# Optimization experiments

Measured on AMD Instinct MI355X. Metric: run time of the kernel, lower is better.

The kernel has to match this reference:

```python
import jax, jax.numpy as jnp
import numpy as np

B, N, C, H = 8, 1024, 768, 12
D = C // H
SCALE = D ** -0.5


def setup_inputs() -> dict:
    key = jax.random.key(0)
    ks = jax.random.split(key, 6)
    std = 0.02
    return {
        "x": jax.random.normal(ks[0], (B, N, C), dtype=jnp.float32),
        "w_qkv": jax.random.normal(ks[1], (3 * C, C), dtype=jnp.float32) * std,
        "w_proj": jax.random.normal(ks[2], (C, C), dtype=jnp.float32) * std,
        "b_proj": jnp.zeros((C,), dtype=jnp.float32),
        "conv_l_w": jax.random.normal(ks[3], (H, H), dtype=jnp.float32) * std,
        "conv_w_w": jax.random.normal(ks[4], (H, H), dtype=jnp.float32) * std,
    }


def reference(x, w_qkv, w_proj, b_proj, conv_l_w, conv_w_w):
    Bx, Nx, Cx = x.shape
    # qkv projection: torch Linear uses x @ W^T
    qkv = (x @ w_qkv.T).reshape(Bx, Nx, 3, H, D)
    qkv = jnp.transpose(qkv, (2, 0, 3, 1, 4))  # [3, B, H, N, D]
    q, k, v = qkv[0], qkv[1], qkv[2]
    q = q * SCALE
    attn = jnp.einsum("bhnd,bhmd->bhnm", q, k)  # [B,H,N,N]
    # 1x1 conv across heads (conv_l)
    attn = jnp.einsum("oh,bhnm->bonm", conv_l_w, attn)
    attn = jax.nn.softmax(attn, axis=-1)
    # 1x1 conv across heads (conv_w)
    attn = jnp.einsum("oh,bhnm->bonm", conv_w_w, attn)
    out = jnp.einsum("bhnm,bhmd->bhnd", attn, v)
    out = jnp.transpose(out, (0, 2, 1, 3)).reshape(Bx, Nx, Cx)
    return out @ w_proj.T + b_proj
```

## Files before the change

### kernel.cpp

```cpp
#include <hip/hip_runtime.h>
#include <hip/hip_bf16.h>

typedef __attribute__((ext_vector_type(8))) short short8;
typedef __attribute__((ext_vector_type(4))) short short4v;
typedef __attribute__((ext_vector_type(4))) float float4v;

#define NB 8
#define NH 12
#define NN 1024
#define ND 64
#define NC 768

#define RAWBAR() do { \
  asm volatile("s_waitcnt lgkmcnt(0)" ::: "memory"); \
  __builtin_amdgcn_s_barrier(); \
} while (0)

__device__ __forceinline__ short f2bf(float f) {
  __hip_bfloat16 h = __float2bfloat16(f);
  union { __hip_bfloat16 h; short s; } u; u.h = h; return u.s;
}
__device__ __forceinline__ unsigned pk2(float a, float b) {
  unsigned ua = (unsigned short)f2bf(a);
  unsigned ub = (unsigned short)f2bf(b);
  return ua | (ub << 16);
}

template<int MODE>
__global__ __launch_bounds__(256, 2)
void gemm_kernel(const void* __restrict__ Ap, const float* __restrict__ Bw,
                 const float* __restrict__ bias,
                 __hip_bfloat16* __restrict__ Qo, __hip_bfloat16* __restrict__ Ko,
                 __hip_bfloat16* __restrict__ VTo, float* __restrict__ Out)
{
  __shared__ short As[128 * 40];
  __shared__ short Bs[128 * 40];
  const int tid = threadIdx.x;
  const int w = tid >> 6, lane = tid & 63, lr = lane & 15, lg = lane >> 4;
  const int wr = w >> 1, wc = w & 1;
  const int n0 = blockIdx.x * 128, m0 = blockIdx.y * 128;

  float4v acc[4][4];
  #pragma unroll
  for (int i = 0; i < 4; i++)
    #pragma unroll
    for (int j = 0; j < 4; j++)
      acc[i][j] = (float4v){0.f, 0.f, 0.f, 0.f};

  for (int kt = 0; kt < 768; kt += 32) {
    if (MODE == 0) {
      const float* A = (const float*)Ap;
      #pragma unroll
      for (int i2 = 0; i2 < 4; i2++) {
        int c = tid + 256 * i2;
        int row = c >> 3, c4 = c & 7;
        float4v v = *(const float4v*)(A + (size_t)(m0 + row) * 768 + kt + c4 * 4);
        short4v s = { f2bf(v[0]), f2bf(v[1]), f2bf(v[2]), f2bf(v[3]) };
        *(short4v*)(&As[row * 40 + c4 * 4]) = s;
      }
    } else {
      const __hip_bfloat16* A = (const __hip_bfloat16*)Ap;
      #pragma unroll
      for (int i2 = 0; i2 < 2; i2++) {
        int c = tid + 256 * i2;
        int row = c >> 2, c8 = c & 3;
        *(short8*)(&As[row * 40 + c8 * 8]) =
            *(const short8*)(A + (size_t)(m0 + row) * 768 + kt + c8 * 8);
      }
    }
    #pragma unroll
    for (int i2 = 0; i2 < 4; i2++) {
      int c = tid + 256 * i2;
      int row = c >> 3, c4 = c & 7;
      float4v v = *(const float4v*)(Bw + (size_t)(n0 + row) * 768 + kt + c4 * 4);
      short4v s = { f2bf(v[0]), f2bf(v[1]), f2bf(v[2]), f2bf(v[3]) };
      *(short4v*)(&Bs[row * 40 + c4 * 4]) = s;
    }
    __syncthreads();

    short8 af[4], bfr[4];
    #pragma unroll
    for (int i = 0; i < 4; i++)
      af[i] = *(const short8*)(&As[(wr * 64 + i * 16 + lr) * 40 + lg * 8]);
    #pragma unroll
    for (int j = 0; j < 4; j++)
      bfr[j] = *(const short8*)(&Bs[(wc * 64 + j * 16 + lr) * 40 + lg * 8]);
    #pragma unroll
    for (int i = 0; i < 4; i++)
      #pragma unroll
      for (int j = 0; j < 4; j++)
        acc[i][j] = __builtin_amdgcn_mfma_f32_16x16x32_bf16(af[i], bfr[j], acc[i][j], 0, 0, 0);
    __syncthreads();
  }

  #pragma unroll
  for (int i = 0; i < 4; i++) {
    #pragma unroll
    for (int j = 0; j < 4; j++) {
      #pragma unroll
      for (int r = 0; r < 4; r++) {
        float val = acc[i][j][r];
        int mg_ = m0 + wr * 64 + i * 16 + lg * 4 + r;
        int ng_ = n0 + wc * 64 + j * 16 + lr;
        if (MODE == 0) {
          int s = ng_ / 768;
          int rem = ng_ - s * 768;
          int h = rem >> 6, d = rem & 63;
          int b = mg_ >> 10, n = mg_ & 1023;
          if (s == 0)
            Qo[(((size_t)b * NH + h) * NN + n) * ND + d] = __float2bfloat16(val * 0.125f);
          else if (s == 1)
            Ko[(((size_t)b * NH + h) * NN + n) * ND + d] = __float2bfloat16(val);
          else
            VTo[(((size_t)b * NH + h) * ND + d) * NN + n] = __float2bfloat16(val);
        } else {
          Out[(size_t)mg_ * NC + ng_] = val + bias[ng_];
        }
      }
    }
  }
}

__global__ __launch_bounds__(256, 2)
void attn_kernel(const __hip_bfloat16* __restrict__ Qg, const __hip_bfloat16* __restrict__ Kg,
                 const __hip_bfloat16* __restrict__ VTg,
                 const float* __restrict__ convl, const float* __restrict__ convw,
                 __hip_bfloat16* __restrict__ AOut)
{
  __shared__ short Sb[18432];
  __shared__ short pm[18688];
  __shared__ short lwA[512];
  __shared__ short wwT[512];

  const int tid = threadIdx.x;
  const int w = tid >> 6, lane = tid & 63, lr = lane & 15, lg = lane >> 4;
  const int b = blockIdx.x & 7;
  const int n0 = (blockIdx.x >> 3) * 16;
  const float4v zf = (float4v){0.f, 0.f, 0.f, 0.f};

  for (int i = tid; i < 512; i += 256) {
    int r = i >> 5, k = i & 31;
    bool v = (r < 12) && (k < 12);
    lwA[i] = v ? f2bf(convl[r * 12 + k]) : (short)0;
    wwT[i] = v ? f2bf(convw[r * 12 + k]) : (short)0;
  }
  for (int i = tid; i < 1024; i += 256) {
    unsigned* p = (unsigned*)(&Sb[i * 18 + 12]);
    p[0] = 0; p[1] = 0; p[2] = 0;
  }

  short8 qf[3][2];
  #pragma unroll
  for (int hh = 0; hh < 3; hh++)
    #pragma unroll
    for (int ks = 0; ks < 2; ks++)
      qf[hh][ks] = *(const short8*)(Qg +
          (((size_t)b * NH + w * 3 + hh) * NN + n0 + lr) * ND + ks * 32 + lg * 8);

  short8 kreg[3][2][2];
  auto loadK = [&](int t) {
    #pragma unroll
    for (int hh = 0; hh < 3; hh++) {
      const size_t kbase = (((size_t)b * NH + w * 3 + hh) * NN + t * 32) * ND;
      #pragma unroll
      for (int j = 0; j < 2; j++)
        #pragma unroll
        for (int ks = 0; ks < 2; ks++)
          kreg[hh][j][ks] = *(const short8*)(Kg + kbase +
              (size_t)(j * 16 + lr) * ND + ks * 32 + lg * 8);
    }
  };

  auto qkStep = [&](int buf) {
    #pragma unroll
    for (int hh = 0; hh < 3; hh++) {
      const int h = w * 3 + hh;
      #pragma unroll
      for (int j = 0; j < 2; j++) {
        float4v a = __builtin_amdgcn_mfma_f32_16x16x32_bf16(qf[hh][0], kreg[hh][j][0], zf, 0, 0, 0);
        a = __builtin_amdgcn_mfma_f32_16x16x32_bf16(qf[hh][1], kreg[hh][j][1], a, 0, 0, 0);
        #pragma unroll
        for (int r = 0; r < 4; r++)
          Sb[(buf * 32 + (lg * 4 + r) * 2 + j) * 288 + lr * 18 + h] = f2bf(a[r]);
      }
    }
  };

  loadK(0);
  RAWBAR();
  const short8 lwf = *(const short8*)(&lwA[lr * 32 + lg * 8]);
  const short8 wwf = *(const short8*)(&wwT[lr * 32 + lg * 8]);

  float Lacc[4][4];
  #pragma unroll
  for (int r = 0; r < 4; r++)
    #pragma unroll
    for (int nn = 0; nn < 4; nn++) Lacc[r][nn] = 0.f;

  for (int t = 0; t <= 32; t++) {
    __builtin_amdgcn_s_setprio(1);
    if (t < 32) qkStep(t & 1);
    __builtin_amdgcn_s_setprio(0);
    if (t < 32) loadK(t < 31 ? t + 1 : 0);
    if (t >= 1) {
      const int buf = (t - 1) & 1;
      #pragma unroll
      for (int cc = 0; cc < 8; cc++) {
        const int c = w * 8 + cc;
        short8 sb = *(const short8*)(&Sb[(buf * 32 + c) * 288 + lr * 18 + lg * 8]);
        float4v d = __builtin_amdgcn_mfma_f32_16x16x32_bf16(lwf, sb, zf, 0, 0, 0);
        #pragma unroll
        for (int r = 0; r < 4; r++)
          Lacc[r][cc >> 1] += __expf(d[r]);
      }
    }
    RAWBAR();
  }
  float logLreg[4][4];
  #pragma unroll
  for (int r = 0; r < 4; r++)
    #pragma unroll
    for (int nn = 0; nn < 4; nn++) {
      float v = Lacc[r][nn];
      v += __shfl_xor(v, 1);
      v += __shfl_xor(v, 2);
      v += __shfl_xor(v, 4);
      v += __shfl_xor(v, 8);
      logLreg[r][nn] = __logf(v);
    }

  float4v oacc[3][4];
  #pragma unroll
  for (int hh = 0; hh < 3; hh++)
    #pragma unroll
    for (int jd = 0; jd < 4; jd++) oacc[hh][jd] = zf;

  for (int t = 0; t <= 33; t++) {
    short8 pf[3];
    short8 vt[3][4];
    if (t >= 2) {
      const int pb = t & 1;
      const int m0v = (t - 2) * 32;
      #pragma unroll
      for (int hh = 0; hh < 3; hh++) {
        const int o2 = w * 3 + hh;
        pf[hh] = *(const short8*)(&pm[pb * 9344 + o2 * 584 + lr * 36 + lg * 8]);
        const size_t vbase = ((size_t)b * NH + o2) * ND * NN;
        #pragma unroll
        for (int jd = 0; jd < 4; jd++)
          vt[hh][jd] = *(const short8*)(VTg + vbase +
              (size_t)(jd * 16 + lr) * NN + m0v + lg * 8);
      }
    }
    __builtin_amdgcn_s_setprio(1);
    if (t < 32) {
      qkStep(t & 1);
      if (t < 31) loadK(t + 1);
    }
    __builtin_amdgcn_s_setprio(0);
    if (t >= 1 && t <= 32) {
      const int buf = (t - 1) & 1;
      #pragma unroll
      for (int cc = 0; cc < 8; cc++) {
        const int c = w * 8 + cc;
        short8 sb = *(const short8*)(&Sb[(buf * 32 + c) * 288 + lr * 18 + lg * 8]);
        float4v d = __builtin_amdgcn_mfma_f32_16x16x32_bf16(lwf, sb, zf, 0, 0, 0);
        float p0 = __expf(d[0] - logLreg[0][cc >> 1]);
        float p1 = __expf(d[1] - logLreg[1][cc >> 1]);
        float p2 = __expf(d[2] - logLreg[2][cc >> 1]);
        float p3 = __expf(d[3] - logLreg[3][cc >> 1]);
        unsigned* dst = (unsigned*)(&Sb[(buf * 32 + c) * 288 + lr * 18 + lg * 4]);
        dst[0] = pk2(p0, p1);
        dst[1] = pk2(p2, p3);
      }
      asm volatile("s_waitcnt lgkmcnt(0)" ::: "memory");
      __builtin_amdgcn_sched_barrier(0);
      #pragma unroll
      for (int cc = 0; cc < 8; cc++) {
        const int c = w * 8 + cc;
        short8 pb2 = *(const short8*)(&Sb[(buf * 32 + c) * 288 + lr * 18 + lg * 8]);
        float4v d = __builtin_amdgcn_mfma_f32_16x16x32_bf16(pb2, wwf, zf, 0, 0, 0);
        unsigned* dst = (unsigned*)(&pm[buf * 9344 + lr * 584 + (c >> 1) * 36 + (c & 1) * 16 + lg * 4]);
        dst[0] = pk2(d[0], d[1]);
        dst[1] = pk2(d[2], d[3]);
      }
    }
    if (t >= 2) {
      __builtin_amdgcn_s_setprio(1);
      #pragma unroll
      for (int hh = 0; hh < 3; hh++)
        #pragma unroll
        for (int jd = 0; jd < 4; jd++)
          oacc[hh][jd] = __builtin_amdgcn_mfma_f32_16x16x32_bf16(vt[hh][jd], pf[hh], oacc[hh][jd], 0, 0, 0);
      __builtin_amdgcn_s_setprio(0);
    }
    RAWBAR();
  }

  #pragma unroll
  for (int hh = 0; hh < 3; hh++) {
    const int o2 = w * 3 + hh;
    #pragma unroll
    for (int jd = 0; jd < 4; jd++) {
      size_t base = ((size_t)b * NN + n0 + lr) * NC + o2 * 64 + jd * 16 + lg * 4;
      unsigned* dst = (unsigned*)(&AOut[base]);
      dst[0] = pk2(oacc[hh][jd][0], oacc[hh][jd][1]);
      dst[1] = pk2(oacc[hh][jd][2], oacc[hh][jd][3]);
    }
  }
}

extern "C" void kernel_launch(void* const* d_in, const int* in_sizes, int n_in,
                              void* d_out, int out_size, void* d_ws, size_t ws_size,
                              hipStream_t stream) {
  const float* x      = (const float*)d_in[0];
  const float* w_qkv  = (const float*)d_in[1];
  const float* w_proj = (const float*)d_in[2];
  const float* b_proj = (const float*)d_in[3];
  const float* conv_l = (const float*)d_in[4];
  const float* conv_w = (const float*)d_in[5];
  float* out = (float*)d_out;

  const size_t NE = (size_t)NB * NH * NN * ND;
  __hip_bfloat16* Qb = (__hip_bfloat16*)d_ws;
  __hip_bfloat16* Kb = Qb + NE;
  __hip_bfloat16* VT = Kb + NE;
  __hip_bfloat16* AO = VT + NE;

  gemm_kernel<0><<<dim3(18, 64), 256, 0, stream>>>(x, w_qkv, nullptr, Qb, Kb, VT, nullptr);
  attn_kernel<<<dim3(512), 256, 0, stream>>>(Qb, Kb, VT, conv_l, conv_w, AO);
  gemm_kernel<1><<<dim3(6, 64), 256, 0, stream>>>(AO, w_proj, b_proj, nullptr, nullptr, nullptr, out);
}
```

Baseline: 377.0 us.

## Process 64-key tiles in first attention pass using a unified shared buffer

```diff
diff --git a/kernel.cpp b/kernel.cpp
--- a/kernel.cpp
+++ b/kernel.cpp
@@ -127,10 +127,11 @@
                  const float* __restrict__ convl, const float* __restrict__ convw,
                  __hip_bfloat16* __restrict__ AOut)
 {
-  __shared__ short Sb[18432];
-  __shared__ short pm[18688];
+  __shared__ short SMEM[37376];
   __shared__ short lwA[512];
   __shared__ short wwT[512];
+  short* Sb = SMEM;
+  short* pm = SMEM + 18688;
 
   const int tid = threadIdx.x;
   const int w = tid >> 6, lane = tid & 63, lr = lane & 15, lg = lane >> 4;
@@ -144,10 +145,7 @@
     lwA[i] = v ? f2bf(convl[r * 12 + k]) : (short)0;
     wwT[i] = v ? f2bf(convw[r * 12 + k]) : (short)0;
   }
-  for (int i = tid; i < 1024; i += 256) {
-    unsigned* p = (unsigned*)(&Sb[i * 18 + 12]);
-    p[0] = 0; p[1] = 0; p[2] = 0;
-  }
+  for (int i = tid; i < 18688; i += 256) ((unsigned*)SMEM)[i] = 0u;
 
   short8 qf[3][2];
   #pragma unroll
@@ -158,31 +156,16 @@
           (((size_t)b * NH + w * 3 + hh) * NN + n0 + lr) * ND + ks * 32 + lg * 8);
 
   short8 kreg[3][2][2];
-  auto loadK = [&](int t) {
+  auto loadK = [&](int mbase) {
     #pragma unroll
     for (int hh = 0; hh < 3; hh++) {
-      const size_t kbase = (((size_t)b * NH + w * 3 + hh) * NN + t * 32) * ND;
+      const size_t kbase = (((size_t)b * NH + w * 3 + hh) * NN + mbase) * ND;
       #pragma unroll
       for (int j = 0; j < 2; j++)
         #pragma unroll
         for (int ks = 0; ks < 2; ks++)
           kreg[hh][j][ks] = *(const short8*)(Kg + kbase +
               (size_t)(j * 16 + lr) * ND + ks * 32 + lg * 8);
-    }
-  };
-
-  auto qkStep = [&](int buf) {
-    #pragma unroll
-    for (int hh = 0; hh < 3; hh++) {
-      const int h = w * 3 + hh;
-      #pragma unroll
-      for (int j = 0; j < 2; j++) {
-        float4v a = __builtin_amdgcn_mfma_f32_16x16x32_bf16(qf[hh][0], kreg[hh][j][0], zf, 0, 0, 0);
-        a = __builtin_amdgcn_mfma_f32_16x16x32_bf16(qf[hh][1], kreg[hh][j][1], a, 0, 0, 0);
-        #pragma unroll
-        for (int r = 0; r < 4; r++)
-          Sb[(buf * 32 + (lg * 4 + r) * 2 + j) * 288 + lr * 18 + h] = f2bf(a[r]);
-      }
     }
   };
 
@@ -197,21 +180,51 @@
     #pragma unroll
     for (int nn = 0; nn < 4; nn++) Lacc[r][nn] = 0.f;
 
-  for (int t = 0; t <= 32; t++) {
+  for (int t = 0; t <= 16; t++) {
     __builtin_amdgcn_s_setprio(1);
-    if (t < 32) qkStep(t & 1);
+    if (t < 16) {
+      const int buf = (t & 1) * 64;
+      const int mt = t * 64;
+      #pragma unroll
+      for (int hh = 0; hh < 3; hh++) {
+        const int h = w * 3 + hh;
+        #pragma unroll
+        for (int j = 0; j < 2; j++) {
+          float4v a = __builtin_amdgcn_mfma_f32_16x16x32_bf16(qf[hh][0], kreg[hh][j][0], zf, 0, 0, 0);
+          a = __builtin_amdgcn_mfma_f32_16x16x32_bf16(qf[hh][1], kreg[hh][j][1], a, 0, 0, 0);
+          #pragma unroll
+          for (int r = 0; r < 4; r++)
+            Sb[(buf + ((lg * 4 + r) * 4 + j)) * 292 + lr * 18 + h] = f2bf(a[r]);
+        }
+      }
+      #pragma unroll
+      for (int hh = 0; hh < 3; hh++) {
+        const int h = w * 3 + hh;
+        const size_t kbase = (((size_t)b * NH + h) * NN + mt + 32) * ND;
+        #pragma unroll
+        for (int j = 0; j < 2; j++) {
+          short8 kb0 = *(const short8*)(Kg + kbase + (size_t)(j * 16 + lr) * ND + lg * 8);
+          short8 kb1 = *(const short8*)(Kg + kbase + (size_t)(j * 16 + lr) * ND + 32 + lg * 8);
+          float4v a = __builtin_amdgcn_mfma_f32_16x16x32_bf16(qf[hh][0], kb0, zf, 0, 0, 0);
+          a = __builtin_amdgcn_mfma_f32_16x16x32_bf16(qf[hh][1], kb1, a, 0, 0, 0);
+          #pragma unroll
+          for (int r = 0; r < 4; r++)
+            Sb[(buf + ((lg * 4 + r) * 4 + 2 + j)) * 292 + lr * 18 + h] = f2bf(a[r]);
+        }
+      }
+      loadK(t < 15 ? (t + 1) * 64 : 0);
+    }
     __builtin_amdgcn_s_setprio(0);
-    if (t < 32) loadK(t < 31 ? t + 1 : 0);
     if (t >= 1) {
-      const int buf = (t - 1) & 1;
-      #pragma unroll
-      for (int cc = 0; cc < 8; cc++) {
-        const int c = w * 8 + cc;
-        short8 sb = *(const short8*)(&Sb[(buf * 32 + c) * 288 + lr * 18 + lg * 8]);
+      const int buf = ((t - 1) & 1) * 64;
+      #pragma unroll
+      for (int cc = 0; cc < 16; cc++) {
+        const int c = w * 16 + cc;
+        short8 sb = *(const short8*)(&Sb[(buf + c) * 292 + lr * 18 + lg * 8]);
         float4v d = __builtin_amdgcn_mfma_f32_16x16x32_bf16(lwf, sb, zf, 0, 0, 0);
         #pragma unroll
         for (int r = 0; r < 4; r++)
-          Lacc[r][cc >> 1] += __expf(d[r]);
+          Lacc[r][cc >> 2] += __expf(d[r]);
       }
     }
     RAWBAR();
@@ -239,12 +252,12 @@
     short8 pf[3];
     short8 vt[3][4];
     if (t >= 2) {
-      const int pb = t & 1;
+      const int pb = (t & 1) * 9344;
       const int m0v = (t - 2) * 32;
       #pragma unroll
       for (int hh = 0; hh < 3; hh++) {
         const int o2 = w * 3 + hh;
-        pf[hh] = *(const short8*)(&pm[pb * 9344 + o2 * 584 + lr * 36 + lg * 8]);
+        pf[hh] = *(const short8*)(&pm[pb + o2 * 584 + lr * 36 + lg * 8]);
         const size_t vbase = ((size_t)b * NH + o2) * ND * NN;
         #pragma unroll
         for (int jd = 0; jd < 4; jd++)
@@ -254,22 +267,34 @@
     }
     __builtin_amdgcn_s_setprio(1);
     if (t < 32) {
-      qkStep(t & 1);
-      if (t < 31) loadK(t + 1);
+      const int buf = (t & 1) * 32;
+      #pragma unroll
+      for (int hh = 0; hh < 3; hh++) {
+        const int h = w * 3 + hh;
+        #pragma unroll
+        for (int j = 0; j < 2; j++) {
+          float4v a = __builtin_amdgcn_mfma_f32_16x16x32_bf16(qf[hh][0], kreg[hh][j][0], zf, 0, 0, 0);
+          a = __builtin_amdgcn_mfma_f32_16x16x32_bf16(qf[hh][1], kreg[hh][j][1], a, 0, 0, 0);
+          #pragma unroll
+          for (int r = 0; r < 4; r++)
+            Sb[(buf + ((lg * 4 + r) * 2 + j)) * 292 + lr * 18 + h] = f2bf(a[r]);
+        }
+      }
+      if (t < 31) loadK((t + 1) * 32);
     }
     __builtin_amdgcn_s_setprio(0);
     if (t >= 1 && t <= 32) {
-      const int buf = (t - 1) & 1;
+      const int buf = ((t - 1) & 1) * 32;
       #pragma unroll
       for (int cc = 0; cc < 8; cc++) {
         const int c = w * 8 + cc;
-        short8 sb = *(const short8*)(&Sb[(buf * 32 + c) * 288 + lr * 18 + lg * 8]);
+        short8 sb = *(const short8*)(&Sb[(buf + c) * 292 + lr * 18 + lg * 8]);
         float4v d = __builtin_amdgcn_mfma_f32_16x16x32_bf16(lwf, sb, zf, 0, 0, 0);
         float p0 = __expf(d[0] - logLreg[0][cc >> 1]);
         float p1 = __expf(d[1] - logLreg[1][cc >> 1]);
         float p2 = __expf(d[2] - logLreg[2][cc >> 1]);
         float p3 = __expf(d[3] - logLreg[3][cc >> 1]);
-        unsigned* dst = (unsigned*)(&Sb[(buf * 32 + c) * 288 + lr * 18 + lg * 4]);
+        unsigned* dst = (unsigned*)(&Sb[(buf + c) * 292 + lr * 18 + lg * 4]);
         dst[0] = pk2(p0, p1);
         dst[1] = pk2(p2, p3);
       }
@@ -278,9 +303,10 @@
       #pragma unroll
       for (int cc = 0; cc < 8; cc++) {
         const int c = w * 8 + cc;
-        short8 pb2 = *(const short8*)(&Sb[(buf * 32 + c) * 288 + lr * 18 + lg * 8]);
+        short8 pb2 = *(const short8*)(&Sb[(buf + c) * 292 + lr * 18 + lg * 8]);
         float4v d = __builtin_amdgcn_mfma_f32_16x16x32_bf16(pb2, wwf, zf, 0, 0, 0);
-        unsigned* dst = (unsigned*)(&pm[buf * 9344 + lr * 584 + (c >> 1) * 36 + (c & 1) * 16 + lg * 4]);
+        unsigned* dst = (unsigned*)(&pm[((t - 1) & 1) * 9344 + lr * 584 +
+                                        (c >> 1) * 36 + (c & 1) * 16 + lg * 4]);
         dst[0] = pk2(d[0], d[1]);
         dst[1] = pk2(d[2], d[3]);
       }
```

Measured after the change: 409.0 us. 1.08x slower.

## Double-buffer K and V register prefetch and pad score buffer rows

Applied to the files above, without the earlier changes.

```diff
diff --git a/kernel.cpp b/kernel.cpp
--- a/kernel.cpp
+++ b/kernel.cpp
@@ -127,7 +127,7 @@
                  const float* __restrict__ convl, const float* __restrict__ convw,
                  __hip_bfloat16* __restrict__ AOut)
 {
-  __shared__ short Sb[18432];
+  __shared__ short Sb[18688];
   __shared__ short pm[18688];
   __shared__ short lwA[512];
   __shared__ short wwT[512];
@@ -144,10 +144,12 @@
     lwA[i] = v ? f2bf(convl[r * 12 + k]) : (short)0;
     wwT[i] = v ? f2bf(convw[r * 12 + k]) : (short)0;
   }
-  for (int i = tid; i < 1024; i += 256) {
-    unsigned* p = (unsigned*)(&Sb[i * 18 + 12]);
-    p[0] = 0; p[1] = 0; p[2] = 0;
-  }
+  for (int i = tid; i < 9344; i += 256) { ((unsigned*)Sb)[i] = 0u; ((unsigned*)pm)[i] = 0u; }
+
+  const int klane = lr * ND + lg * 8;
+  const int vlane = lr * NN + lg * 8;
+  const __hip_bfloat16* Kw = Kg + (((size_t)b * NH + w * 3) * NN) * ND;
+  const __hip_bfloat16* Vw = VTg + (((size_t)b * NH + w * 3) * ND) * NN;
 
   short8 qf[3][2];
   #pragma unroll
@@ -157,36 +159,42 @@
       qf[hh][ks] = *(const short8*)(Qg +
           (((size_t)b * NH + w * 3 + hh) * NN + n0 + lr) * ND + ks * 32 + lg * 8);
 
-  short8 kreg[3][2][2];
-  auto loadK = [&](int t) {
-    #pragma unroll
-    for (int hh = 0; hh < 3; hh++) {
-      const size_t kbase = (((size_t)b * NH + w * 3 + hh) * NN + t * 32) * ND;
+  short8 KA[3][2][2], KB[3][2][2];
+  short8 VA[3][4], VB[3][4];
+
+  auto loadK = [&](int mbase, short8 (&KD)[3][2][2]) {
+    #pragma unroll
+    for (int hh = 0; hh < 3; hh++)
       #pragma unroll
       for (int j = 0; j < 2; j++)
         #pragma unroll
         for (int ks = 0; ks < 2; ks++)
-          kreg[hh][j][ks] = *(const short8*)(Kg + kbase +
-              (size_t)(j * 16 + lr) * ND + ks * 32 + lg * 8);
-    }
-  };
-
-  auto qkStep = [&](int buf) {
+          KD[hh][j][ks] = *(const short8*)(Kw + hh * (NN * ND) +
+              (mbase + j * 16) * ND + ks * 32 + klane);
+  };
+  auto loadVT = [&](int m0v, short8 (&VD)[3][4]) {
+    #pragma unroll
+    for (int hh = 0; hh < 3; hh++)
+      #pragma unroll
+      for (int jd = 0; jd < 4; jd++)
+        VD[hh][jd] = *(const short8*)(Vw + hh * (ND * NN) + jd * 16 * NN + m0v + vlane);
+  };
+  auto qkStep = [&](int bufc, short8 (&KC)[3][2][2]) {
     #pragma unroll
     for (int hh = 0; hh < 3; hh++) {
       const int h = w * 3 + hh;
       #pragma unroll
       for (int j = 0; j < 2; j++) {
-        float4v a = __builtin_amdgcn_mfma_f32_16x16x32_bf16(qf[hh][0], kreg[hh][j][0], zf, 0, 0, 0);
-        a = __builtin_amdgcn_mfma_f32_16x16x32_bf16(qf[hh][1], kreg[hh][j][1], a, 0, 0, 0);
+        float4v a = __builtin_amdgcn_mfma_f32_16x16x32_bf16(qf[hh][0], KC[hh][j][0], zf, 0, 0, 0);
+        a = __builtin_amdgcn_mfma_f32_16x16x32_bf16(qf[hh][1], KC[hh][j][1], a, 0, 0, 0);
         #pragma unroll
         for (int r = 0; r < 4; r++)
-          Sb[(buf * 32 + (lg * 4 + r) * 2 + j) * 288 + lr * 18 + h] = f2bf(a[r]);
+          Sb[(bufc + (lg * 4 + r) * 2 + j) * 292 + lr * 18 + h] = f2bf(a[r]);
       }
     }
   };
 
-  loadK(0);
+  loadK(0, KA);
   RAWBAR();
   const short8 lwf = *(const short8*)(&lwA[lr * 32 + lg * 8]);
   const short8 wwf = *(const short8*)(&wwT[lr * 32 + lg * 8]);
@@ -197,25 +205,33 @@
     #pragma unroll
     for (int nn = 0; nn < 4; nn++) Lacc[r][nn] = 0.f;
 
-  for (int t = 0; t <= 32; t++) {
+  auto convSum = [&](int parity) {
+    const int bufc = parity * 32;
+    #pragma unroll
+    for (int cc = 0; cc < 8; cc++) {
+      const int c = w * 8 + cc;
+      short8 sb = *(const short8*)(&Sb[(bufc + c) * 292 + lr * 18 + lg * 8]);
+      float4v d = __builtin_amdgcn_mfma_f32_16x16x32_bf16(lwf, sb, zf, 0, 0, 0);
+      #pragma unroll
+      for (int r = 0; r < 4; r++)
+        Lacc[r][cc >> 1] += __expf(d[r]);
+    }
+  };
+  auto p1seg = [&](int T, short8 (&KC)[3][2][2], short8 (&KN)[3][2][2]) {
+    loadK(T < 31 ? (T + 1) * 32 : 0, KN);
     __builtin_amdgcn_s_setprio(1);
-    if (t < 32) qkStep(t & 1);
+    qkStep((T & 1) * 32, KC);
     __builtin_amdgcn_s_setprio(0);
-    if (t < 32) loadK(t < 31 ? t + 1 : 0);
-    if (t >= 1) {
-      const int buf = (t - 1) & 1;
-      #pragma unroll
-      for (int cc = 0; cc < 8; cc++) {
-        const int c = w * 8 + cc;
-        short8 sb = *(const short8*)(&Sb[(buf * 32 + c) * 288 + lr * 18 + lg * 8]);
-        float4v d = __builtin_amdgcn_mfma_f32_16x16x32_bf16(lwf, sb, zf, 0, 0, 0);
-        #pragma unroll
-        for (int r = 0; r < 4; r++)
-          Lacc[r][cc >> 1] += __expf(d[r]);
-      }
-    }
+    if (T >= 1) convSum((T - 1) & 1);
     RAWBAR();
-  }
+  };
+  for (int tp = 0; tp < 32; tp += 2) {
+    p1seg(tp, KA, KB);
+    p1seg(tp + 1, KB, KA);
+  }
+  convSum(1);
+  RAWBAR();
+
   float logLreg[4][4];
   #pragma unroll
   for (int r = 0; r < 4; r++)
@@ -235,66 +251,63 @@
     #pragma unroll
     for (int jd = 0; jd < 4; jd++) oacc[hh][jd] = zf;
 
-  for (int t = 0; t <= 33; t++) {
+  auto stream2 = [&](int tau) {
+    const int bufc = (tau & 1) * 32;
+    const int pmb = (tau & 1) * 9344;
+    #pragma unroll
+    for (int cc = 0; cc < 8; cc++) {
+      const int c = w * 8 + cc;
+      short8 sb = *(const short8*)(&Sb[(bufc + c) * 292 + lr * 18 + lg * 8]);
+      float4v d = __builtin_amdgcn_mfma_f32_16x16x32_bf16(lwf, sb, zf, 0, 0, 0);
+      float p0 = __expf(d[0] - logLreg[0][cc >> 1]);
+      float p1 = __expf(d[1] - logLreg[1][cc >> 1]);
+      float p2 = __expf(d[2] - logLreg[2][cc >> 1]);
+      float p3 = __expf(d[3] - logLreg[3][cc >> 1]);
+      unsigned* dst = (unsigned*)(&Sb[(bufc + c) * 292 + lr * 18 + lg * 4]);
+      dst[0] = pk2(p0, p1);
+      dst[1] = pk2(p2, p3);
+    }
+    asm volatile("s_waitcnt lgkmcnt(0)" ::: "memory");
+    __builtin_amdgcn_sched_barrier(0);
+    #pragma unroll
+    for (int cc = 0; cc < 8; cc++) {
+      const int c = w * 8 + cc;
+      short8 pb2 = *(const short8*)(&Sb[(bufc + c) * 292 + lr * 18 + lg * 8]);
+      float4v d = __builtin_amdgcn_mfma_f32_16x16x32_bf16(pb2, wwf, zf, 0, 0, 0);
+      unsigned* dst = (unsigned*)(&pm[pmb + lr * 584 + (c >> 1) * 36 + (c & 1) * 16 + lg * 4]);
+      dst[0] = pk2(d[0], d[1]);
+      dst[1] = pk2(d[2], d[3]);
+    }
+  };
+
+  auto p2seg = [&](int T, short8 (&VLD)[3][4], short8 (&VUSE)[3][4]) {
     short8 pf[3];
-    short8 vt[3][4];
-    if (t >= 2) {
-      const int pb = t & 1;
-      const int m0v = (t - 2) * 32;
-      #pragma unroll
-      for (int hh = 0; hh < 3; hh++) {
-        const int o2 = w * 3 + hh;
-        pf[hh] = *(const short8*)(&pm[pb * 9344 + o2 * 584 + lr * 36 + lg * 8]);
-        const size_t vbase = ((size_t)b * NH + o2) * ND * NN;
-        #pragma unroll
-        for (int jd = 0; jd < 4; jd++)
-          vt[hh][jd] = *(const short8*)(VTg + vbase +
-              (size_t)(jd * 16 + lr) * NN + m0v + lg * 8);
-      }
-    }
+    if (T >= 2) {
+      const int pmb = (T & 1) * 9344;
+      #pragma unroll
+      for (int hh = 0; hh < 3; hh++)
+        pf[hh] = *(const short8*)(&pm[pmb + (w * 3 + hh) * 584 + lr * 36 + lg * 8]);
+    }
+    if (T >= 1 && T <= 32) loadVT((T - 1) * 32, VLD);
     __builtin_amdgcn_s_setprio(1);
-    if (t < 32) {
-      qkStep(t & 1);
-      if (t < 31) loadK(t + 1);
-    }
+    if (T < 32) qkStep((T & 1) * 32, KA);
     __builtin_amdgcn_s_setprio(0);
-    if (t >= 1 && t <= 32) {
-      const int buf = (t - 1) & 1;
-      #pragma unroll
-      for (int cc = 0; cc < 8; cc++) {
-        const int c = w * 8 + cc;
-        short8 sb = *(const short8*)(&Sb[(buf * 32 + c) * 288 + lr * 18 + lg * 8]);
-        float4v d = __builtin_amdgcn_mfma_f32_16x16x32_bf16(lwf, sb, zf, 0, 0, 0);
-        float p0 = __expf(d[0] - logLreg[0][cc >> 1]);
-        float p1 = __expf(d[1] - logLreg[1][cc >> 1]);
-        float p2 = __expf(d[2] - logLreg[2][cc >> 1]);
-        float p3 = __expf(d[3] - logLreg[3][cc >> 1]);
-        unsigned* dst = (unsigned*)(&Sb[(buf * 32 + c) * 288 + lr * 18 + lg * 4]);
-        dst[0] = pk2(p0, p1);
-        dst[1] = pk2(p2, p3);
-      }
-      asm volatile("s_waitcnt lgkmcnt(0)" ::: "memory");
-      __builtin_amdgcn_sched_barrier(0);
-      #pragma unroll
-      for (int cc = 0; cc < 8; cc++) {
-        const int c = w * 8 + cc;
-        short8 pb2 = *(const short8*)(&Sb[(buf * 32 + c) * 288 + lr * 18 + lg * 8]);
-        float4v d = __builtin_amdgcn_mfma_f32_16x16x32_bf16(pb2, wwf, zf, 0, 0, 0);
-        unsigned* dst = (unsigned*)(&pm[buf * 9344 + lr * 584 + (c >> 1) * 36 + (c & 1) * 16 + lg * 4]);
-        dst[0] = pk2(d[0], d[1]);
-        dst[1] = pk2(d[2], d[3]);
-      }
-    }
-    if (t >= 2) {
+    if (T < 31) loadK((T + 1) * 32, KA);
+    if (T >= 1 && T <= 32) stream2(T - 1);
+    if (T >= 2) {
       __builtin_amdgcn_s_setprio(1);
       #pragma unroll
       for (int hh = 0; hh < 3; hh++)
         #pragma unroll
         for (int jd = 0; jd < 4; jd++)
-          oacc[hh][jd] = __builtin_amdgcn_mfma_f32_16x16x32_bf16(vt[hh][jd], pf[hh], oacc[hh][jd], 0, 0, 0);
+          oacc[hh][jd] = __builtin_amdgcn_mfma_f32_16x16x32_bf16(VUSE[hh][jd], pf[hh], oacc[hh][jd], 0, 0, 0);
       __builtin_amdgcn_s_setprio(0);
     }
     RAWBAR();
+  };
+  for (int tp = 0; tp < 34; tp += 2) {
+    p2seg(tp, VB, VA);
+    p2seg(tp + 1, VA, VB);
   }
 
   #pragma unroll
```

Result: slower. 438.8 us (+16.4%).

## Split attention into L-pass and PV-pass kernels, storing exp scores in workspace

Applied to the files above, without the earlier changes.

```diff
diff --git a/kernel.cpp b/kernel.cpp
--- a/kernel.cpp
+++ b/kernel.cpp
@@ -4,6 +4,7 @@
 typedef __attribute__((ext_vector_type(8))) short short8;
 typedef __attribute__((ext_vector_type(4))) short short4v;
 typedef __attribute__((ext_vector_type(4))) float float4v;
+typedef __attribute__((ext_vector_type(2))) unsigned uint2v;
 
 #define NB 8
 #define NH 12
@@ -122,15 +123,12 @@
 }
 
 __global__ __launch_bounds__(256, 2)
-void attn_kernel(const __hip_bfloat16* __restrict__ Qg, const __hip_bfloat16* __restrict__ Kg,
-                 const __hip_bfloat16* __restrict__ VTg,
-                 const float* __restrict__ convl, const float* __restrict__ convw,
-                 __hip_bfloat16* __restrict__ AOut)
+void attn_l_kernel(const __hip_bfloat16* __restrict__ Qg, const __hip_bfloat16* __restrict__ Kg,
+                   const float* __restrict__ convl,
+                   short* __restrict__ Pg, float* __restrict__ Lg)
 {
-  __shared__ short Sb[18432];
-  __shared__ short pm[18688];
+  __shared__ short Sb[18688];
   __shared__ short lwA[512];
-  __shared__ short wwT[512];
 
   const int tid = threadIdx.x;
   const int w = tid >> 6, lane = tid & 63, lr = lane & 15, lg = lane >> 4;
@@ -140,14 +138,9 @@
 
   for (int i = tid; i < 512; i += 256) {
     int r = i >> 5, k = i & 31;
-    bool v = (r < 12) && (k < 12);
-    lwA[i] = v ? f2bf(convl[r * 12 + k]) : (short)0;
-    wwT[i] = v ? f2bf(convw[r * 12 + k]) : (short)0;
-  }
-  for (int i = tid; i < 1024; i += 256) {
-    unsigned* p = (unsigned*)(&Sb[i * 18 + 12]);
-    p[0] = 0; p[1] = 0; p[2] = 0;
-  }
+    lwA[i] = (r < 12 && k < 12) ? f2bf(convl[r * 12 + k]) : (short)0;
+  }
+  for (int i = tid; i < 9344; i += 256) ((unsigned*)Sb)[i] = 0u;
 
   short8 qf[3][2];
   #pragma unroll
@@ -171,25 +164,11 @@
     }
   };
 
-  auto qkStep = [&](int buf) {
-    #pragma unroll
-    for (int hh = 0; hh < 3; hh++) {
-      const int h = w * 3 + hh;
-      #pragma unroll
-      for (int j = 0; j < 2; j++) {
-        float4v a = __builtin_amdgcn_mfma_f32_16x16x32_bf16(qf[hh][0], kreg[hh][j][0], zf, 0, 0, 0);
-        a = __builtin_amdgcn_mfma_f32_16x16x32_bf16(qf[hh][1], kreg[hh][j][1], a, 0, 0, 0);
-        #pragma unroll
-        for (int r = 0; r < 4; r++)
-          Sb[(buf * 32 + (lg * 4 + r) * 2 + j) * 288 + lr * 18 + h] = f2bf(a[r]);
-      }
-    }
-  };
+  short* Pblk = Pg + (size_t)blockIdx.x * 32 * 6144;
 
   loadK(0);
   RAWBAR();
   const short8 lwf = *(const short8*)(&lwA[lr * 32 + lg * 8]);
-  const short8 wwf = *(const short8*)(&wwT[lr * 32 + lg * 8]);
 
   float Lacc[4][4];
   #pragma unroll
@@ -199,24 +178,45 @@
 
   for (int t = 0; t <= 32; t++) {
     __builtin_amdgcn_s_setprio(1);
-    if (t < 32) qkStep(t & 1);
+    if (t < 32) {
+      const int bufc = (t & 1) * 32;
+      #pragma unroll
+      for (int hh = 0; hh < 3; hh++) {
+        const int h = w * 3 + hh;
+        #pragma unroll
+        for (int j = 0; j < 2; j++) {
+          float4v a = __builtin_amdgcn_mfma_f32_16x16x32_bf16(qf[hh][0], kreg[hh][j][0], zf, 0, 0, 0);
+          a = __builtin_amdgcn_mfma_f32_16x16x32_bf16(qf[hh][1], kreg[hh][j][1], a, 0, 0, 0);
+          #pragma unroll
+          for (int r = 0; r < 4; r++)
+            Sb[(bufc + (lg * 4 + r) * 2 + j) * 292 + lr * 18 + h] = f2bf(a[r]);
+        }
+      }
+      if (t < 31) loadK(t + 1);
+    }
     __builtin_amdgcn_s_setprio(0);
-    if (t < 32) loadK(t < 31 ? t + 1 : 0);
     if (t >= 1) {
-      const int buf = (t - 1) & 1;
+      const int bufc = ((t - 1) & 1) * 32;
+      short* Pt = Pblk + (size_t)(t - 1) * 6144;
       #pragma unroll
       for (int cc = 0; cc < 8; cc++) {
         const int c = w * 8 + cc;
-        short8 sb = *(const short8*)(&Sb[(buf * 32 + c) * 288 + lr * 18 + lg * 8]);
+        short8 sb = *(const short8*)(&Sb[(bufc + c) * 292 + lr * 18 + lg * 8]);
         float4v d = __builtin_amdgcn_mfma_f32_16x16x32_bf16(lwf, sb, zf, 0, 0, 0);
-        #pragma unroll
-        for (int r = 0; r < 4; r++)
-          Lacc[r][cc >> 1] += __expf(d[r]);
+        float e0 = __expf(d[0]), e1 = __expf(d[1]);
+        float e2 = __expf(d[2]), e3 = __expf(d[3]);
+        Lacc[0][cc >> 1] += e0; Lacc[1][cc >> 1] += e1;
+        Lacc[2][cc >> 1] += e2; Lacc[3][cc >> 1] += e3;
+        if (lg < 3) {
+          uint2v st = { pk2(e0, e1), pk2(e2, e3) };
+          int soff = (lg < 2) ? (lr * 8 + lg * 4) : (128 + lr * 4);
+          *(uint2v*)(Pt + (size_t)c * 192 + soff) = st;
+        }
       }
     }
     RAWBAR();
   }
-  float logLreg[4][4];
+
   #pragma unroll
   for (int r = 0; r < 4; r++)
     #pragma unroll
@@ -226,8 +226,58 @@
       v += __shfl_xor(v, 2);
       v += __shfl_xor(v, 4);
       v += __shfl_xor(v, 8);
-      logLreg[r][nn] = __logf(v);
-    }
+      int o = lg * 4 + r;
+      if (lr == 0 && o < 12)
+        Lg[((size_t)b * NH + o) * NN + n0 + w * 4 + nn] = 1.0f / v;
+    }
+}
+
+__global__ __launch_bounds__(256, 1)
+void attn_pv_kernel(const __hip_bfloat16* __restrict__ VTg, const float* __restrict__ convw,
+                    const float* __restrict__ Lg, const short* __restrict__ Pg,
+                    __hip_bfloat16* __restrict__ AOut)
+{
+  __shared__ short pm[18688];
+
+  const int tid = threadIdx.x;
+  const int w = tid >> 6, lane = tid & 63, lr = lane & 15, lg = lane >> 4;
+  const int b = blockIdx.x & 7;
+  const int n0 = (blockIdx.x >> 3) * 16;
+  const float4v zf = (float4v){0.f, 0.f, 0.f, 0.f};
+
+  short8 wwS[4];
+  #pragma unroll
+  for (int nn = 0; nn < 4; nn++) {
+    const int n = n0 + w * 4 + nn;
+    #pragma unroll
+    for (int j = 0; j < 8; j++) {
+      const int o = lg * 8 + j;
+      float wv = (lr < 12 && o < 12) ? convw[lr * 12 + o] : 0.f;
+      float iv = (o < 12) ? Lg[((size_t)b * NH + o) * NN + n] : 0.f;
+      wwS[nn][j] = f2bf(wv * iv);
+    }
+  }
+
+  const short* Pblk = Pg + (size_t)blockIdx.x * 32 * 6144;
+  const __hip_bfloat16* Vw = VTg + (((size_t)b * NH + w * 3) * ND) * NN;
+  const int vlane = lr * NN + lg * 8;
+
+  short8 PA[8], PB[8];
+  auto loadP = [&](int t, short8 (&PD)[8]) {
+    const short* Pt = Pblk + (size_t)t * 6144;
+    #pragma unroll
+    for (int cc = 0; cc < 8; cc++) {
+      const int c = w * 8 + cc;
+      short8 v = (short8)(short)0;
+      if (lg == 0) {
+        v = *(const short8*)(Pt + (size_t)c * 192 + lr * 8);
+      } else if (lg == 1) {
+        short4v t4 = *(const short4v*)(Pt + (size_t)c * 192 + 128 + lr * 4);
+        v[0] = t4[0]; v[1] = t4[1]; v[2] = t4[2]; v[3] = t4[3];
+      }
+      PD[cc] = v;
+    }
+  };
 
   float4v oacc[3][4];
   #pragma unroll
@@ -235,57 +285,36 @@
     #pragma unroll
     for (int jd = 0; jd < 4; jd++) oacc[hh][jd] = zf;
 
-  for (int t = 0; t <= 33; t++) {
+  auto seg = [&](int T, short8 (&Pcur)[8], short8 (&Pnext)[8]) {
     short8 pf[3];
     short8 vt[3][4];
-    if (t >= 2) {
-      const int pb = t & 1;
-      const int m0v = (t - 2) * 32;
-      #pragma unroll
-      for (int hh = 0; hh < 3; hh++) {
-        const int o2 = w * 3 + hh;
-        pf[hh] = *(const short8*)(&pm[pb * 9344 + o2 * 584 + lr * 36 + lg * 8]);
-        const size_t vbase = ((size_t)b * NH + o2) * ND * NN;
+    if (T >= 1) {
+      const int pmb = ((T - 1) & 1) * 9344;
+      #pragma unroll
+      for (int hh = 0; hh < 3; hh++)
+        pf[hh] = *(const short8*)(&pm[pmb + (w * 3 + hh) * 584 + lr * 36 + lg * 8]);
+      const int m0v = (T - 1) * 32;
+      #pragma unroll
+      for (int hh = 0; hh < 3; hh++)
         #pragma unroll
         for (int jd = 0; jd < 4; jd++)
-          vt[hh][jd] = *(const short8*)(VTg + vbase +
-              (size_t)(jd * 16 + lr) * NN + m0v + lg * 8);
-      }
-    }
-    __builtin_amdgcn_s_setprio(1);
-    if (t < 32) {
-      qkStep(t & 1);
-      if (t < 31) loadK(t + 1);
-    }
-    __builtin_amdgcn_s_setprio(0);
-    if (t >= 1 && t <= 32) {
-      const int buf = (t - 1) & 1;
+          vt[hh][jd] = *(const short8*)(Vw + hh * (ND * NN) + jd * 16 * NN + m0v + vlane);
+    }
+    if (T + 1 < 32) loadP(T + 1, Pnext);
+    if (T < 32) {
+      const int pmb = (T & 1) * 9344;
+      __builtin_amdgcn_s_setprio(1);
       #pragma unroll
       for (int cc = 0; cc < 8; cc++) {
         const int c = w * 8 + cc;
-        short8 sb = *(const short8*)(&Sb[(buf * 32 + c) * 288 + lr * 18 + lg * 8]);
-        float4v d = __builtin_amdgcn_mfma_f32_16x16x32_bf16(lwf, sb, zf, 0, 0, 0);
-        float p0 = __expf(d[0] - logLreg[0][cc >> 1]);
-        float p1 = __expf(d[1] - logLreg[1][cc >> 1]);
-        float p2 = __expf(d[2] - logLreg[2][cc >> 1]);
-        float p3 = __expf(d[3] - logLreg[3][cc >> 1]);
-        unsigned* dst = (unsigned*)(&Sb[(buf * 32 + c) * 288 + lr * 18 + lg * 4]);
-        dst[0] = pk2(p0, p1);
-        dst[1] = pk2(p2, p3);
-      }
-      asm volatile("s_waitcnt lgkmcnt(0)" ::: "memory");
-      __builtin_amdgcn_sched_barrier(0);
-      #pragma unroll
-      for (int cc = 0; cc < 8; cc++) {
-        const int c = w * 8 + cc;
-        short8 pb2 = *(const short8*)(&Sb[(buf * 32 + c) * 288 + lr * 18 + lg * 8]);
-        float4v d = __builtin_amdgcn_mfma_f32_16x16x32_bf16(pb2, wwf, zf, 0, 0, 0);
-        unsigned* dst = (unsigned*)(&pm[buf * 9344 + lr * 584 + (c >> 1) * 36 + (c & 1) * 16 + lg * 4]);
+        float4v d = __builtin_amdgcn_mfma_f32_16x16x32_bf16(Pcur[cc], wwS[cc >> 1], zf, 0, 0, 0);
+        unsigned* dst = (unsigned*)(&pm[pmb + lr * 584 + (c >> 1) * 36 + (c & 1) * 16 + lg * 4]);
         dst[0] = pk2(d[0], d[1]);
         dst[1] = pk2(d[2], d[3]);
       }
-    }
-    if (t >= 2) {
+      __builtin_amdgcn_s_setprio(0);
+    }
+    if (T >= 1) {
       __builtin_amdgcn_s_setprio(1);
       #pragma unroll
       for (int hh = 0; hh < 3; hh++)
@@ -295,6 +324,12 @@
       __builtin_amdgcn_s_setprio(0);
     }
     RAWBAR();
+  };
+
+  loadP(0, PA);
+  for (int tp = 0; tp <= 32; tp += 2) {
+    seg(tp, PA, PB);
+    if (tp + 1 <= 32) seg(tp + 1, PB, PA);
   }
 
   #pragma unroll
@@ -326,8 +361,11 @@
   __hip_bfloat16* Kb = Qb + NE;
   __hip_bfloat16* VT = Kb + NE;
   __hip_bfloat16* AO = VT + NE;
+  float* Lg = (float*)(AO + NE);
+  short* Pg = (short*)(Lg + (size_t)NB * NH * NN);
 
   gemm_kernel<0><<<dim3(18, 64), 256, 0, stream>>>(x, w_qkv, nullptr, Qb, Kb, VT, nullptr);
-  attn_kernel<<<dim3(512), 256, 0, stream>>>(Qb, Kb, VT, conv_l, conv_w, AO);
+  attn_l_kernel<<<dim3(512), 256, 0, stream>>>(Qb, Kb, conv_l, Pg, Lg);
+  attn_pv_kernel<<<dim3(512), 256, 0, stream>>>(VT, conv_w, Lg, Pg, AO);
   gemm_kernel<1><<<dim3(6, 64), 256, 0, stream>>>(AO, w_proj, b_proj, nullptr, nullptr, nullptr, out);
 }
```

After: 483.7 us. 1.28x slower.
